# Kernel tuning notes

Measured on AMD Instinct MI355X. Metric: run time of the kernel, lower is better.

The kernel has to match this reference:

```python
import jax, jax.numpy as jnp
import numpy as np
from functools import partial

# ---- constants mirroring init_kwargs ----
T, B, J, I = 1024, 32, 128, 512
KD = 16              # max_delay (dilated kernel size)
THETA = 1.0          # threshold
SIG = 0.5            # delay.SIG, frozen (requires_grad=False)
ALPHA = 5.0          # ATan surrogate alpha
EPS = 1e-5           # BatchNorm eps

# ---- ATan surrogate spike (spikingjelly): fwd = heaviside, bwd = atan grad ----
@jax.custom_vjp
def atan_spike(x):
    return (x >= 0).astype(x.dtype)

def _atan_fwd(x):
    return atan_spike(x), x

def _atan_bwd(x, g):
    return (g * (ALPHA / 2.0) / (1.0 + (jnp.pi / 2.0 * ALPHA * x) ** 2),)

atan_spike.defvjp(_atan_fwd, _atan_bwd)

def _dcls_kernel(w, P):
    # DCLS1d 'gauss' version, kernel_count=1: gaussian bump centered at P + KD//2,
    # normalized over the kernel axis, scaled by weight. w,P: (I,J) -> (I,J,KD)
    c = P + KD // 2
    k = jnp.arange(KD, dtype=w.dtype)                        # (KD,)
    g = jnp.exp(-0.5 * ((k[None, None, :] - c[:, :, None]) / SIG) ** 2)
    g = g / (g.sum(-1, keepdims=True) + 1e-7)
    return w[:, :, None] * g                                  # (I,J,KD)

def setup_inputs() -> dict:
    key = jax.random.key(0)
    ks = jax.random.split(key, 6)
    x = jax.random.normal(ks[0], (T, B, J), dtype=jnp.float32)
    # kaiming_uniform_ fan_in = J*1 -> bound = sqrt(6/fan_in)
    bound = float(np.sqrt(6.0 / J))
    delay_w = jax.random.uniform(ks[1], (I, J), jnp.float32, -bound, bound)
    # P ~ U(-max_delay//2, max_delay//2), then clamped (already in range)
    delay_P = jax.random.uniform(ks[2], (I, J), jnp.float32, -(KD // 2), KD // 2)
    beta = jax.random.uniform(ks[3], (I,), jnp.float32, 0.0, 1.0)
    bn_gamma = jnp.ones((I,), jnp.float32)
    bn_beta = jnp.zeros((I,), jnp.float32)
    U0 = jax.random.uniform(ks[4], (B, I), jnp.float32)       # RandomBatchwiseInit(0,1)
    return {"x": x, "delay_w": delay_w, "delay_P": delay_P, "beta": beta,
            "bn_gamma": bn_gamma, "bn_beta": bn_beta, "U0": U0}

def reference(x, delay_w, delay_P, beta, bn_gamma, bn_beta, U0):
    # --- delayed conv: (T,B,J) -> (B,J,T) -> left-pad KD-1 -> conv1d -> (T,B,I) ---
    xb = jnp.transpose(x, (1, 2, 0))                          # (B,J,T)
    xb = jnp.pad(xb, ((0, 0), (0, 0), (KD - 1, 0)))           # (B,J,T+KD-1)
    kern = _dcls_kernel(delay_w, delay_P)                     # (I,J,KD)
    y = jax.lax.conv_general_dilated(
        xb, kern, window_strides=(1,), padding='VALID',
        dimension_numbers=('NCH', 'OIH', 'NCH'))              # (B,I,T)
    y = jnp.transpose(y, (2, 0, 1))                           # (T,B,I)

    # --- BatchNorm1d over reshaped (T*B, I, 1): stats over T*B per channel ---
    yf = y.reshape(T * B, I)
    mean = yf.mean(axis=0)
    var = yf.var(axis=0)
    yf = (yf - mean) * jax.lax.rsqrt(var + EPS) * bn_gamma + bn_beta
    y = yf.reshape(T, B, I)

    # --- soft-reset LIF scan (NOTE: original passes RAW beta, not sigmoid(beta)) ---
    def step(carry, xt):
        Ut, St = carry
        Ut = beta * (Ut - THETA * St) + (1.0 - beta) * xt
        St = atan_spike(Ut - THETA)
        return (Ut, St), St

    S0 = jnp.zeros_like(U0)
    _, o = jax.lax.scan(step, (U0, S0), y)                    # (T,B,I)
    return o
```

## Files before the change

### kernel.cpp

```cpp
#include <hip/hip_runtime.h>

#define TT 1024
#define NB 32
#define NJ 128
#define NI 512
#define KD 16
#define LVL 1048576

typedef short bf16x8 __attribute__((ext_vector_type(8)));
typedef float floatx4 __attribute__((ext_vector_type(4)));

struct S3 { short h, m, l; };

__device__ __forceinline__ S3 split3(float v) {
    S3 o;
    unsigned hb = __float_as_uint(v) & 0xFFFF0000u;
    float hf = __uint_as_float(hb);
    float r1 = v - hf;
    unsigned mb = __float_as_uint(r1) & 0xFFFF0000u;
    float mf = __uint_as_float(mb);
    float r2 = r1 - mf;
    unsigned lb = __float_as_uint(r2) & 0xFFFF0000u;
    o.h = (short)(hb >> 16);
    o.m = (short)(mb >> 16);
    o.l = (short)(lb >> 16);
    return o;
}

__global__ __launch_bounds__(256) void dcls_kern(const float* __restrict__ w,
                                                 const float* __restrict__ P,
                                                 short* __restrict__ WF) {
    int idx = blockIdx.x * 256 + threadIdx.x;
    int j = idx & (NJ - 1);
    int i = idx >> 7;
    float wv = w[i * NJ + j];
    float c  = P[i * NJ + j] + (float)(KD / 2);
    float g[KD];
    float s = 0.f;
#pragma unroll
    for (int k = 0; k < KD; ++k) {
        float u = (float)k - c;
        g[k] = expf(-2.0f * u * u);
        s += g[k];
    }
    float inv = wv / (s + 1e-7f);
    size_t base = (size_t)(i >> 4) * 32768 + (size_t)(j >> 3) * 128 + (i & 15) * 8 + (j & 7);
#pragma unroll
    for (int d = 0; d < KD; ++d) {
        S3 sp = split3(g[(KD - 1) - d] * inv);
        size_t off = base + (size_t)d * 2048;
        WF[off]           = sp.h;
        WF[off + LVL]     = sp.m;
        WF[off + 2 * LVL] = sp.l;
    }
}

__global__ __launch_bounds__(512, 2) void conv_mfma(const float* __restrict__ x,
                                                    const short* __restrict__ WF,
                                                    float* __restrict__ y) {
    __shared__ __align__(16) short PA[256][64];
    __shared__ __align__(16) short PL[256][64];

    const int t0 = blockIdx.x * 256;
    const int i0 = blockIdx.y * 256;
    const int b  = blockIdx.z;
    const int tid = threadIdx.x;

    const int ch   = tid & 3;
    const int rw   = tid >> 2;
    const int l    = tid & 63;
    const int wv   = tid >> 6;
    const int lr16 = l & 15;
    const int kb   = l >> 4;
    const int wm   = wv >> 2;
    const int wn   = wv & 3;

    const short* pnf[4];
#pragma unroll
    for (int nf = 0; nf < 4; ++nf) {
        int ig = (i0 + wn * 64 + nf * 16) >> 4;
        pnf[nf] = WF + (size_t)ig * 32768 + l * 8;
    }

    floatx4 acc[8][4];
#pragma unroll
    for (int mf = 0; mf < 8; ++mf)
#pragma unroll
        for (int nf = 0; nf < 4; ++nf)
#pragma unroll
            for (int e = 0; e < 4; ++e) acc[mf][nf][e] = 0.f;

    float4 ga[2][2];
    bf16x8 Wh[4], Wm[4], Wl[4];

#define LOADW(K) {                                                              \
    int koff = ((((K) >> 2) * 16 + ((K) & 3) * 4)) * 128;                       \
    _Pragma("unroll") for (int nf = 0; nf < 4; ++nf) {                          \
        const short* p = pnf[nf] + koff;                                        \
        Wh[nf] = *(const bf16x8*)(p);                                           \
        Wm[nf] = *(const bf16x8*)(p + LVL);                                     \
        Wl[nf] = *(const bf16x8*)(p + 2 * LVL); } }

#define LOADX(K) {                                                              \
    int dn = (K) >> 2, j0n = ((K) & 3) << 5;                                    \
    _Pragma("unroll") for (int s = 0; s < 2; ++s) {                             \
        int t = t0 + rw + s * 128 - dn;                                         \
        float4 z4 = make_float4(0.f, 0.f, 0.f, 0.f);                            \
        ga[s][0] = z4; ga[s][1] = z4;                                           \
        if (t >= 0) {                                                           \
            const float* ax = x + ((size_t)t * NB + b) * NJ + j0n + ch * 8;     \
            ga[s][0] = *(const float4*)ax;                                      \
            ga[s][1] = *(const float4*)(ax + 4); } } }

#define STAGEW() {                                                              \
    _Pragma("unroll") for (int s = 0; s < 2; ++s) {                             \
        int r = rw + s * 128;                                                   \
        int key = r & 7;                                                        \
        char* rowA = (char*)PA + r * 128;                                       \
        char* rowL = (char*)PL + r * 128;                                       \
        S3 a0 = split3(ga[s][0].x), a1 = split3(ga[s][0].y),                    \
           a2 = split3(ga[s][0].z), a3 = split3(ga[s][0].w),                    \
           a4 = split3(ga[s][1].x), a5 = split3(ga[s][1].y),                    \
           a6 = split3(ga[s][1].z), a7 = split3(ga[s][1].w);                    \
        bf16x8 h8, m8, l8;                                                      \
        h8[0]=a0.h; h8[1]=a1.h; h8[2]=a2.h; h8[3]=a3.h;                         \
        h8[4]=a4.h; h8[5]=a5.h; h8[6]=a6.h; h8[7]=a7.h;                         \
        m8[0]=a0.m; m8[1]=a1.m; m8[2]=a2.m; m8[3]=a3.m;                         \
        m8[4]=a4.m; m8[5]=a5.m; m8[6]=a6.m; m8[7]=a7.m;                         \
        l8[0]=a0.l; l8[1]=a1.l; l8[2]=a2.l; l8[3]=a3.l;                         \
        l8[4]=a4.l; l8[5]=a5.l; l8[6]=a6.l; l8[7]=a7.l;                         \
        *(bf16x8*)(rowA + ((ch ^ key) * 16))       = h8;                        \
        *(bf16x8*)(rowA + (((ch + 4) ^ key) * 16)) = m8;                        \
        *(bf16x8*)(rowL + ((ch ^ key) * 16))       = l8; } }

#define DOMFMA() {                                                              \
    _Pragma("unroll") for (int mf = 0; mf < 8; ++mf) {                          \
        int row = wm * 128 + mf * 16 + lr16;                                    \
        int key = row & 7;                                                      \
        const char* rowA = (const char*)PA + row * 128;                         \
        const char* rowL = (const char*)PL + row * 128;                         \
        bf16x8 ah = *(const bf16x8*)(rowA + ((kb ^ key) * 16));                 \
        bf16x8 am = *(const bf16x8*)(rowA + (((kb + 4) ^ key) * 16));           \
        bf16x8 al = *(const bf16x8*)(rowL + ((kb ^ key) * 16));                 \
        _Pragma("unroll") for (int nf = 0; nf < 4; ++nf)                        \
            acc[mf][nf] = __builtin_amdgcn_mfma_f32_16x16x32_bf16(ah, Wh[nf], acc[mf][nf], 0, 0, 0); \
        _Pragma("unroll") for (int nf = 0; nf < 4; ++nf)                        \
            acc[mf][nf] = __builtin_amdgcn_mfma_f32_16x16x32_bf16(ah, Wm[nf], acc[mf][nf], 0, 0, 0); \
        _Pragma("unroll") for (int nf = 0; nf < 4; ++nf)                        \
            acc[mf][nf] = __builtin_amdgcn_mfma_f32_16x16x32_bf16(am, Wh[nf], acc[mf][nf], 0, 0, 0); \
        _Pragma("unroll") for (int nf = 0; nf < 4; ++nf)                        \
            acc[mf][nf] = __builtin_amdgcn_mfma_f32_16x16x32_bf16(am, Wm[nf], acc[mf][nf], 0, 0, 0); \
        _Pragma("unroll") for (int nf = 0; nf < 4; ++nf)                        \
            acc[mf][nf] = __builtin_amdgcn_mfma_f32_16x16x32_bf16(ah, Wl[nf], acc[mf][nf], 0, 0, 0); \
        _Pragma("unroll") for (int nf = 0; nf < 4; ++nf)                        \
            acc[mf][nf] = __builtin_amdgcn_mfma_f32_16x16x32_bf16(al, Wh[nf], acc[mf][nf], 0, 0, 0); \
    } }

    LOADX(0)

#pragma unroll 1
    for (int kk = 0; kk < 64; ++kk) {
        __syncthreads();
        STAGEW()
        __syncthreads();
        if (kk + 1 < 64) { LOADX(kk + 1) }
        LOADW(kk)
        DOMFMA()
    }
#undef LOADW
#undef LOADX
#undef STAGEW
#undef DOMFMA

#pragma unroll
    for (int mf = 0; mf < 8; ++mf)
#pragma unroll
        for (int nf = 0; nf < 4; ++nf) {
            int ic = i0 + wn * 64 + nf * 16 + lr16;
#pragma unroll
            for (int q = 0; q < 4; ++q) {
                int t = t0 + wm * 128 + mf * 16 + kb * 4 + q;
                y[((size_t)t * NB + b) * NI + ic] = acc[mf][nf][q];
            }
        }
}

__global__ __launch_bounds__(256) void red1(const float* __restrict__ y,
                                            float* __restrict__ part) {
    int r0 = blockIdx.x * 128;
    int c  = threadIdx.x;
    float s0 = 0.f, q0 = 0.f, s1 = 0.f, q1 = 0.f;
#pragma unroll 4
    for (int r = 0; r < 128; ++r) {
        float v0 = y[(size_t)(r0 + r) * NI + c];
        float v1 = y[(size_t)(r0 + r) * NI + c + 256];
        s0 += v0; q0 = fmaf(v0, v0, q0);
        s1 += v1; q1 = fmaf(v1, v1, q1);
    }
    part[blockIdx.x * NI + c]            = s0;
    part[blockIdx.x * NI + c + 256]      = s1;
    part[256 * NI + blockIdx.x * NI + c]       = q0;
    part[256 * NI + blockIdx.x * NI + c + 256] = q1;
}

__global__ __launch_bounds__(512) void red2(const float* __restrict__ part,
                                            const float* __restrict__ gamma,
                                            const float* __restrict__ bbeta,
                                            float* __restrict__ sb) {
    int c = threadIdx.x;
    double s = 0.0, q = 0.0;
#pragma unroll 8
    for (int p = 0; p < 256; ++p) {
        s += (double)part[p * NI + c];
        q += (double)part[256 * NI + p * NI + c];
    }
    double mean = s / 32768.0;
    double var  = q / 32768.0 - mean * mean;
    double scale = (double)gamma[c] / sqrt(var + 1e-5);
    sb[c]      = (float)scale;
    sb[NI + c] = (float)((double)bbeta[c] - mean * scale);
}

__global__ __launch_bounds__(64) void scan_kern(float* __restrict__ y,
                                                const float* __restrict__ sb,
                                                const float* __restrict__ beta,
                                                const float* __restrict__ U0) {
    int g = blockIdx.x * 64 + threadIdx.x;
    int i = g & (NI - 1);
    float scale = sb[i];
    float bias  = sb[NI + i];
    float bet = beta[i];
    float omb = 1.f - bet;
    float u = U0[g];
    float s = 0.f;
    float* yp = y + g;

    float A[32], Bv[32];
#pragma unroll
    for (int r = 0; r < 32; ++r) A[r] = yp[(size_t)r * 16384];

    for (int t0 = 0; t0 < TT; t0 += 64) {
#pragma unroll
        for (int r = 0; r < 32; ++r) Bv[r] = yp[(size_t)(t0 + 32 + r) * 16384];
#pragma unroll
        for (int r = 0; r < 32; ++r) {
            float z = fmaf(A[r], scale, bias);
            u = fmaf(bet, u - s, omb * z);
            s = (u >= 1.f) ? 1.f : 0.f;
            yp[(size_t)(t0 + r) * 16384] = s;
        }
        if (t0 + 64 < TT) {
#pragma unroll
            for (int r = 0; r < 32; ++r) A[r] = yp[(size_t)(t0 + 64 + r) * 16384];
        }
#pragma unroll
        for (int r = 0; r < 32; ++r) {
            float z = fmaf(Bv[r], scale, bias);
            u = fmaf(bet, u - s, omb * z);
            s = (u >= 1.f) ? 1.f : 0.f;
            yp[(size_t)(t0 + 32 + r) * 16384] = s;
        }
    }
}

extern "C" void kernel_launch(void* const* d_in, const int* in_sizes, int n_in,
                              void* d_out, int out_size, void* d_ws, size_t ws_size,
                              hipStream_t stream) {
    const float* x       = (const float*)d_in[0];
    const float* delay_w = (const float*)d_in[1];
    const float* delay_P = (const float*)d_in[2];
    const float* beta    = (const float*)d_in[3];
    const float* bn_g    = (const float*)d_in[4];
    const float* bn_b    = (const float*)d_in[5];
    const float* U0      = (const float*)d_in[6];
    float* y = (float*)d_out;

    short* WF   = (short*)d_ws;
    float* part = (float*)d_ws;
    float* sb   = (float*)d_ws + 2 * 256 * NI;

    dcls_kern<<<dim3(NI * NJ / 256), dim3(256), 0, stream>>>(delay_w, delay_P, WF);
    conv_mfma<<<dim3(TT / 256, NI / 256, NB), dim3(512), 0, stream>>>(x, WF, y);
    red1<<<dim3(TT * NB / 128), dim3(256), 0, stream>>>(y, part);
    red2<<<dim3(1), dim3(512), 0, stream>>>(part, bn_g, bn_b, sb);
    scan_kern<<<dim3(NB * NI / 64), dim3(64), 0, stream>>>(y, sb, beta, U0);
}
```

Before: 357.4 us.

## Double-buffer conv tiles via direct global-to-LDS loads on a pre-padded input

A new kernel copies x into a zero-padded buffer in workspace, so the conv kernel needs no boundary checks. The conv kernel then streams raw fp32 tiles straight into LDS with global_load_lds and double-buffers both the x tiles and the weight registers, overlapping loads with MFMA work. The three-way bf16 split of activations moves from the staging step to each MFMA read. This removes the register round-trip and one barrier per step, but repeats the split for every wave that reads a row and adds one extra kernel pass over x.

```diff
diff --git a/kernel.cpp b/kernel.cpp
--- a/kernel.cpp
+++ b/kernel.cpp
@@ -6,6 +6,8 @@
 #define NI 512
 #define KD 16
 #define LVL 1048576
+#define XPROWS 1039
+#define XPF4 1063936
 
 typedef short bf16x8 __attribute__((ext_vector_type(8)));
 typedef float floatx4 __attribute__((ext_vector_type(4)));
@@ -27,6 +29,12 @@
     return o;
 }
 
+__device__ __forceinline__ void gload16(const void* g, void* l) {
+    __builtin_amdgcn_global_load_lds(
+        (const __attribute__((address_space(1))) void*)g,
+        (__attribute__((address_space(3))) void*)l, 16, 0, 0);
+}
+
 __global__ __launch_bounds__(256) void dcls_kern(const float* __restrict__ w,
                                                  const float* __restrict__ P,
                                                  short* __restrict__ WF) {
@@ -55,19 +63,27 @@
     }
 }
 
-__global__ __launch_bounds__(512, 2) void conv_mfma(const float* __restrict__ x,
+__global__ __launch_bounds__(512) void pad_kern(const float* __restrict__ x,
+                                                float* __restrict__ xp) {
+    size_t i4 = (size_t)blockIdx.x * 512 + threadIdx.x;
+    if (i4 >= XPF4) return;
+    size_t off = i4 * 4;
+    float4 v = make_float4(0.f, 0.f, 0.f, 0.f);
+    if (off >= (size_t)15 * 4096) v = *(const float4*)(x + off - 61440);
+    *(float4*)(xp + off) = v;
+}
+
+__global__ __launch_bounds__(512, 2) void conv_mfma(const float* __restrict__ xpad,
                                                     const short* __restrict__ WF,
                                                     float* __restrict__ y) {
-    __shared__ __align__(16) short PA[256][64];
-    __shared__ __align__(16) short PL[256][64];
+    __shared__ __align__(16) float XT0[256][32];
+    __shared__ __align__(16) float XT1[256][32];
 
     const int t0 = blockIdx.x * 256;
     const int i0 = blockIdx.y * 256;
     const int b  = blockIdx.z;
     const int tid = threadIdx.x;
 
-    const int ch   = tid & 3;
-    const int rw   = tid >> 2;
     const int l    = tid & 63;
     const int wv   = tid >> 6;
     const int lr16 = l & 15;
@@ -75,6 +91,9 @@
     const int wm   = wv >> 2;
     const int wn   = wv & 3;
 
+    const int srow = tid >> 3;
+    const int gch  = (tid & 7) ^ ((tid >> 3) & 7);
+
     const short* pnf[4];
 #pragma unroll
     for (int nf = 0; nf < 4; ++nf) {
@@ -90,86 +109,72 @@
 #pragma unroll
             for (int e = 0; e < 4; ++e) acc[mf][nf][e] = 0.f;
 
-    float4 ga[2][2];
-    bf16x8 Wh[4], Wm[4], Wl[4];
-
-#define LOADW(K) {                                                              \
+    bf16x8 W0h[4], W0m[4], W0l[4], W1h[4], W1m[4], W1l[4];
+
+#define LOADW(K, H, M, L_) {                                                    \
     int koff = ((((K) >> 2) * 16 + ((K) & 3) * 4)) * 128;                       \
     _Pragma("unroll") for (int nf = 0; nf < 4; ++nf) {                          \
         const short* p = pnf[nf] + koff;                                        \
-        Wh[nf] = *(const bf16x8*)(p);                                           \
-        Wm[nf] = *(const bf16x8*)(p + LVL);                                     \
-        Wl[nf] = *(const bf16x8*)(p + 2 * LVL); } }
-
-#define LOADX(K) {                                                              \
+        H[nf]  = *(const bf16x8*)(p);                                           \
+        M[nf]  = *(const bf16x8*)(p + LVL);                                     \
+        L_[nf] = *(const bf16x8*)(p + 2 * LVL); } }
+
+#define GLOAD(K, TILE) {                                                        \
     int dn = (K) >> 2, j0n = ((K) & 3) << 5;                                    \
-    _Pragma("unroll") for (int s = 0; s < 2; ++s) {                             \
-        int t = t0 + rw + s * 128 - dn;                                         \
-        float4 z4 = make_float4(0.f, 0.f, 0.f, 0.f);                            \
-        ga[s][0] = z4; ga[s][1] = z4;                                           \
-        if (t >= 0) {                                                           \
-            const float* ax = x + ((size_t)t * NB + b) * NJ + j0n + ch * 8;     \
-            ga[s][0] = *(const float4*)ax;                                      \
-            ga[s][1] = *(const float4*)(ax + 4); } } }
-
-#define STAGEW() {                                                              \
-    _Pragma("unroll") for (int s = 0; s < 2; ++s) {                             \
-        int r = rw + s * 128;                                                   \
-        int key = r & 7;                                                        \
-        char* rowA = (char*)PA + r * 128;                                       \
-        char* rowL = (char*)PL + r * 128;                                       \
-        S3 a0 = split3(ga[s][0].x), a1 = split3(ga[s][0].y),                    \
-           a2 = split3(ga[s][0].z), a3 = split3(ga[s][0].w),                    \
-           a4 = split3(ga[s][1].x), a5 = split3(ga[s][1].y),                    \
-           a6 = split3(ga[s][1].z), a7 = split3(ga[s][1].w);                    \
-        bf16x8 h8, m8, l8;                                                      \
-        h8[0]=a0.h; h8[1]=a1.h; h8[2]=a2.h; h8[3]=a3.h;                         \
-        h8[4]=a4.h; h8[5]=a5.h; h8[6]=a6.h; h8[7]=a7.h;                         \
-        m8[0]=a0.m; m8[1]=a1.m; m8[2]=a2.m; m8[3]=a3.m;                         \
-        m8[4]=a4.m; m8[5]=a5.m; m8[6]=a6.m; m8[7]=a7.m;                         \
-        l8[0]=a0.l; l8[1]=a1.l; l8[2]=a2.l; l8[3]=a3.l;                         \
-        l8[4]=a4.l; l8[5]=a5.l; l8[6]=a6.l; l8[7]=a7.l;                         \
-        *(bf16x8*)(rowA + ((ch ^ key) * 16))       = h8;                        \
-        *(bf16x8*)(rowA + (((ch + 4) ^ key) * 16)) = m8;                        \
-        *(bf16x8*)(rowL + ((ch ^ key) * 16))       = l8; } }
-
-#define DOMFMA() {                                                              \
+    _Pragma("unroll") for (int q = 0; q < 4; ++q) {                             \
+        int r  = q * 64 + srow;                                                 \
+        int tp = t0 + r - dn + 15;                                              \
+        const float* src = xpad + ((size_t)tp * NB + b) * NJ + j0n + gch * 4;   \
+        gload16(src, (char*)&TILE[0][0] + q * 8192 + tid * 16); } }
+
+#define DOMFMA(TILE, WH, WM, WL) {                                              \
     _Pragma("unroll") for (int mf = 0; mf < 8; ++mf) {                          \
         int row = wm * 128 + mf * 16 + lr16;                                    \
-        int key = row & 7;                                                      \
-        const char* rowA = (const char*)PA + row * 128;                         \
-        const char* rowL = (const char*)PL + row * 128;                         \
-        bf16x8 ah = *(const bf16x8*)(rowA + ((kb ^ key) * 16));                 \
-        bf16x8 am = *(const bf16x8*)(rowA + (((kb + 4) ^ key) * 16));           \
-        bf16x8 al = *(const bf16x8*)(rowL + ((kb ^ key) * 16));                 \
-        _Pragma("unroll") for (int nf = 0; nf < 4; ++nf)                        \
-            acc[mf][nf] = __builtin_amdgcn_mfma_f32_16x16x32_bf16(ah, Wh[nf], acc[mf][nf], 0, 0, 0); \
-        _Pragma("unroll") for (int nf = 0; nf < 4; ++nf)                        \
-            acc[mf][nf] = __builtin_amdgcn_mfma_f32_16x16x32_bf16(ah, Wm[nf], acc[mf][nf], 0, 0, 0); \
-        _Pragma("unroll") for (int nf = 0; nf < 4; ++nf)                        \
-            acc[mf][nf] = __builtin_amdgcn_mfma_f32_16x16x32_bf16(am, Wh[nf], acc[mf][nf], 0, 0, 0); \
-        _Pragma("unroll") for (int nf = 0; nf < 4; ++nf)                        \
-            acc[mf][nf] = __builtin_amdgcn_mfma_f32_16x16x32_bf16(am, Wm[nf], acc[mf][nf], 0, 0, 0); \
-        _Pragma("unroll") for (int nf = 0; nf < 4; ++nf)                        \
-            acc[mf][nf] = __builtin_amdgcn_mfma_f32_16x16x32_bf16(ah, Wl[nf], acc[mf][nf], 0, 0, 0); \
-        _Pragma("unroll") for (int nf = 0; nf < 4; ++nf)                        \
-            acc[mf][nf] = __builtin_amdgcn_mfma_f32_16x16x32_bf16(al, Wh[nf], acc[mf][nf], 0, 0, 0); \
+        int key = lr16 & 7;                                                     \
+        const float* rp = &TILE[row][0];                                        \
+        int c0 = (((2 * kb)     ^ key) << 2);                                   \
+        int c1 = (((2 * kb + 1) ^ key) << 2);                                   \
+        float4 fa = *(const float4*)(rp + c0);                                  \
+        float4 fb = *(const float4*)(rp + c1);                                  \
+        S3 s0 = split3(fa.x), s1 = split3(fa.y), s2 = split3(fa.z),             \
+           s3 = split3(fa.w), s4 = split3(fb.x), s5 = split3(fb.y),             \
+           s6 = split3(fb.z), s7 = split3(fb.w);                                \
+        bf16x8 ah, am, al;                                                      \
+        ah[0]=s0.h; ah[1]=s1.h; ah[2]=s2.h; ah[3]=s3.h;                         \
+        ah[4]=s4.h; ah[5]=s5.h; ah[6]=s6.h; ah[7]=s7.h;                         \
+        am[0]=s0.m; am[1]=s1.m; am[2]=s2.m; am[3]=s3.m;                         \
+        am[4]=s4.m; am[5]=s5.m; am[6]=s6.m; am[7]=s7.m;                         \
+        al[0]=s0.l; al[1]=s1.l; al[2]=s2.l; al[3]=s3.l;                         \
+        al[4]=s4.l; al[5]=s5.l; al[6]=s6.l; al[7]=s7.l;                         \
+        _Pragma("unroll") for (int nf = 0; nf < 4; ++nf)                        \
+            acc[mf][nf] = __builtin_amdgcn_mfma_f32_16x16x32_bf16(ah, WH[nf], acc[mf][nf], 0, 0, 0); \
+        _Pragma("unroll") for (int nf = 0; nf < 4; ++nf)                        \
+            acc[mf][nf] = __builtin_amdgcn_mfma_f32_16x16x32_bf16(ah, WM[nf], acc[mf][nf], 0, 0, 0); \
+        _Pragma("unroll") for (int nf = 0; nf < 4; ++nf)                        \
+            acc[mf][nf] = __builtin_amdgcn_mfma_f32_16x16x32_bf16(am, WH[nf], acc[mf][nf], 0, 0, 0); \
+        _Pragma("unroll") for (int nf = 0; nf < 4; ++nf)                        \
+            acc[mf][nf] = __builtin_amdgcn_mfma_f32_16x16x32_bf16(am, WM[nf], acc[mf][nf], 0, 0, 0); \
+        _Pragma("unroll") for (int nf = 0; nf < 4; ++nf)                        \
+            acc[mf][nf] = __builtin_amdgcn_mfma_f32_16x16x32_bf16(ah, WL[nf], acc[mf][nf], 0, 0, 0); \
+        _Pragma("unroll") for (int nf = 0; nf < 4; ++nf)                        \
+            acc[mf][nf] = __builtin_amdgcn_mfma_f32_16x16x32_bf16(al, WH[nf], acc[mf][nf], 0, 0, 0); \
     } }
 
-    LOADX(0)
+    GLOAD(0, XT0)
+    LOADW(0, W0h, W0m, W0l)
+    __syncthreads();
 
 #pragma unroll 1
-    for (int kk = 0; kk < 64; ++kk) {
+    for (int kk = 0; kk < 64; kk += 2) {
+        if (kk + 1 < 64) { GLOAD(kk + 1, XT1) LOADW(kk + 1, W1h, W1m, W1l) }
+        DOMFMA(XT0, W0h, W0m, W0l)
         __syncthreads();
-        STAGEW()
+        if (kk + 2 < 64) { GLOAD(kk + 2, XT0) LOADW(kk + 2, W0h, W0m, W0l) }
+        if (kk + 1 < 64) { DOMFMA(XT1, W1h, W1m, W1l) }
         __syncthreads();
-        if (kk + 1 < 64) { LOADX(kk + 1) }
-        LOADW(kk)
-        DOMFMA()
     }
 #undef LOADW
-#undef LOADX
-#undef STAGEW
+#undef GLOAD
 #undef DOMFMA
 
 #pragma unroll
@@ -276,11 +281,13 @@
     float* y = (float*)d_out;
 
     short* WF   = (short*)d_ws;
+    float* xpad = (float*)d_ws + 3 * (size_t)LVL / 2;
     float* part = (float*)d_ws;
     float* sb   = (float*)d_ws + 2 * 256 * NI;
 
     dcls_kern<<<dim3(NI * NJ / 256), dim3(256), 0, stream>>>(delay_w, delay_P, WF);
-    conv_mfma<<<dim3(TT / 256, NI / 256, NB), dim3(512), 0, stream>>>(x, WF, y);
+    pad_kern<<<dim3((XPF4 + 511) / 512), dim3(512), 0, stream>>>(x, xpad);
+    conv_mfma<<<dim3(TT / 256, NI / 256, NB), dim3(512), 0, stream>>>(xpad, WF, y);
     red1<<<dim3(TT * NB / 128), dim3(256), 0, stream>>>(y, part);
     red2<<<dim3(1), dim3(512), 0, stream>>>(part, bn_g, bn_b, sb);
     scan_kern<<<dim3(NB * NI / 64), dim3(64), 0, stream>>>(y, sb, beta, U0);
```

Result: slower. 392.1 us (+9.7%).

## Double-buffer conv LDS tiles and weight registers with interleaved staging

Applied to the files above, without the earlier changes.

Restructures the conv MFMA main loop into a software pipeline. The LDS A/L tiles and the weight register fragments are double-buffered, and the staging of the next tile, the weight loads and the x loads are interleaved between groups of MFMAs. This cuts the two barriers per iteration to one and hides global and LDS latency behind compute. The L tile also uses an 80-byte padded row in place of the XOR swizzle. In exchange the kernel needs 104 KB of dynamic LDS, which may allow only one block per CU where the launch bounds ask for two, and it holds twice as many weight registers.

```diff
diff --git a/kernel.cpp b/kernel.cpp
--- a/kernel.cpp
+++ b/kernel.cpp
@@ -58,8 +58,10 @@
 __global__ __launch_bounds__(512, 2) void conv_mfma(const float* __restrict__ x,
                                                     const short* __restrict__ WF,
                                                     float* __restrict__ y) {
-    __shared__ __align__(16) short PA[256][64];
-    __shared__ __align__(16) short PL[256][64];
+    extern __shared__ __align__(16) char lds[];
+    char* PAb[2]; char* PLb[2];
+    PAb[0] = lds;            PAb[1] = lds + 32768;
+    PLb[0] = lds + 65536;    PLb[1] = lds + 86016;
 
     const int t0 = blockIdx.x * 256;
     const int i0 = blockIdx.y * 256;
@@ -91,15 +93,15 @@
             for (int e = 0; e < 4; ++e) acc[mf][nf][e] = 0.f;
 
     float4 ga[2][2];
-    bf16x8 Wh[4], Wm[4], Wl[4];
-
-#define LOADW(K) {                                                              \
+    bf16x8 W0h[4], W0m[4], W0l[4], W1h[4], W1m[4], W1l[4];
+
+#define LOADW(K, H, M, L_) {                                                    \
     int koff = ((((K) >> 2) * 16 + ((K) & 3) * 4)) * 128;                       \
     _Pragma("unroll") for (int nf = 0; nf < 4; ++nf) {                          \
         const short* p = pnf[nf] + koff;                                        \
-        Wh[nf] = *(const bf16x8*)(p);                                           \
-        Wm[nf] = *(const bf16x8*)(p + LVL);                                     \
-        Wl[nf] = *(const bf16x8*)(p + 2 * LVL); } }
+        H[nf]  = *(const bf16x8*)(p);                                           \
+        M[nf]  = *(const bf16x8*)(p + LVL);                                     \
+        L_[nf] = *(const bf16x8*)(p + 2 * LVL); } }
 
 #define LOADX(K) {                                                              \
     int dn = (K) >> 2, j0n = ((K) & 3) << 5;                                    \
@@ -112,65 +114,77 @@
             ga[s][0] = *(const float4*)ax;                                      \
             ga[s][1] = *(const float4*)(ax + 4); } } }
 
-#define STAGEW() {                                                              \
-    _Pragma("unroll") for (int s = 0; s < 2; ++s) {                             \
-        int r = rw + s * 128;                                                   \
-        int key = r & 7;                                                        \
-        char* rowA = (char*)PA + r * 128;                                       \
-        char* rowL = (char*)PL + r * 128;                                       \
-        S3 a0 = split3(ga[s][0].x), a1 = split3(ga[s][0].y),                    \
-           a2 = split3(ga[s][0].z), a3 = split3(ga[s][0].w),                    \
-           a4 = split3(ga[s][1].x), a5 = split3(ga[s][1].y),                    \
-           a6 = split3(ga[s][1].z), a7 = split3(ga[s][1].w);                    \
-        bf16x8 h8, m8, l8;                                                      \
-        h8[0]=a0.h; h8[1]=a1.h; h8[2]=a2.h; h8[3]=a3.h;                         \
-        h8[4]=a4.h; h8[5]=a5.h; h8[6]=a6.h; h8[7]=a7.h;                         \
-        m8[0]=a0.m; m8[1]=a1.m; m8[2]=a2.m; m8[3]=a3.m;                         \
-        m8[4]=a4.m; m8[5]=a5.m; m8[6]=a6.m; m8[7]=a7.m;                         \
-        l8[0]=a0.l; l8[1]=a1.l; l8[2]=a2.l; l8[3]=a3.l;                         \
-        l8[4]=a4.l; l8[5]=a5.l; l8[6]=a6.l; l8[7]=a7.l;                         \
-        *(bf16x8*)(rowA + ((ch ^ key) * 16))       = h8;                        \
-        *(bf16x8*)(rowA + (((ch + 4) ^ key) * 16)) = m8;                        \
-        *(bf16x8*)(rowL + ((ch ^ key) * 16))       = l8; } }
-
-#define DOMFMA() {                                                              \
-    _Pragma("unroll") for (int mf = 0; mf < 8; ++mf) {                          \
+#define STAGE_ROW(S, BA, BL) {                                                  \
+    int r = rw + (S) * 128;                                                     \
+    int key = r & 7;                                                            \
+    char* rowA = (BA) + r * 128;                                                \
+    char* rowL = (BL) + r * 80;                                                 \
+    S3 a0 = split3(ga[S][0].x), a1 = split3(ga[S][0].y),                        \
+       a2 = split3(ga[S][0].z), a3 = split3(ga[S][0].w),                        \
+       a4 = split3(ga[S][1].x), a5 = split3(ga[S][1].y),                        \
+       a6 = split3(ga[S][1].z), a7 = split3(ga[S][1].w);                        \
+    bf16x8 h8, m8, l8;                                                          \
+    h8[0]=a0.h; h8[1]=a1.h; h8[2]=a2.h; h8[3]=a3.h;                             \
+    h8[4]=a4.h; h8[5]=a5.h; h8[6]=a6.h; h8[7]=a7.h;                             \
+    m8[0]=a0.m; m8[1]=a1.m; m8[2]=a2.m; m8[3]=a3.m;                             \
+    m8[4]=a4.m; m8[5]=a5.m; m8[6]=a6.m; m8[7]=a7.m;                             \
+    l8[0]=a0.l; l8[1]=a1.l; l8[2]=a2.l; l8[3]=a3.l;                             \
+    l8[4]=a4.l; l8[5]=a5.l; l8[6]=a6.l; l8[7]=a7.l;                             \
+    *(bf16x8*)(rowA + ((ch ^ key) * 16))       = h8;                            \
+    *(bf16x8*)(rowA + (((ch + 4) ^ key) * 16)) = m8;                            \
+    *(bf16x8*)(rowL + ch * 16)                 = l8; }
+
+#define DOQUAD(Q, BA, BL, WH, WM, WL) {                                         \
+    _Pragma("unroll") for (int mf = 2 * (Q); mf < 2 * (Q) + 2; ++mf) {          \
         int row = wm * 128 + mf * 16 + lr16;                                    \
         int key = row & 7;                                                      \
-        const char* rowA = (const char*)PA + row * 128;                         \
-        const char* rowL = (const char*)PL + row * 128;                         \
+        const char* rowA = (const char*)(BA) + row * 128;                       \
+        const char* rowL = (const char*)(BL) + row * 80;                        \
         bf16x8 ah = *(const bf16x8*)(rowA + ((kb ^ key) * 16));                 \
         bf16x8 am = *(const bf16x8*)(rowA + (((kb + 4) ^ key) * 16));           \
-        bf16x8 al = *(const bf16x8*)(rowL + ((kb ^ key) * 16));                 \
-        _Pragma("unroll") for (int nf = 0; nf < 4; ++nf)                        \
-            acc[mf][nf] = __builtin_amdgcn_mfma_f32_16x16x32_bf16(ah, Wh[nf], acc[mf][nf], 0, 0, 0); \
-        _Pragma("unroll") for (int nf = 0; nf < 4; ++nf)                        \
-            acc[mf][nf] = __builtin_amdgcn_mfma_f32_16x16x32_bf16(ah, Wm[nf], acc[mf][nf], 0, 0, 0); \
-        _Pragma("unroll") for (int nf = 0; nf < 4; ++nf)                        \
-            acc[mf][nf] = __builtin_amdgcn_mfma_f32_16x16x32_bf16(am, Wh[nf], acc[mf][nf], 0, 0, 0); \
-        _Pragma("unroll") for (int nf = 0; nf < 4; ++nf)                        \
-            acc[mf][nf] = __builtin_amdgcn_mfma_f32_16x16x32_bf16(am, Wm[nf], acc[mf][nf], 0, 0, 0); \
-        _Pragma("unroll") for (int nf = 0; nf < 4; ++nf)                        \
-            acc[mf][nf] = __builtin_amdgcn_mfma_f32_16x16x32_bf16(ah, Wl[nf], acc[mf][nf], 0, 0, 0); \
-        _Pragma("unroll") for (int nf = 0; nf < 4; ++nf)                        \
-            acc[mf][nf] = __builtin_amdgcn_mfma_f32_16x16x32_bf16(al, Wh[nf], acc[mf][nf], 0, 0, 0); \
+        bf16x8 al = *(const bf16x8*)(rowL + kb * 16);                           \
+        _Pragma("unroll") for (int nf = 0; nf < 4; ++nf)                        \
+            acc[mf][nf] = __builtin_amdgcn_mfma_f32_16x16x32_bf16(ah, WH[nf], acc[mf][nf], 0, 0, 0); \
+        _Pragma("unroll") for (int nf = 0; nf < 4; ++nf)                        \
+            acc[mf][nf] = __builtin_amdgcn_mfma_f32_16x16x32_bf16(ah, WM[nf], acc[mf][nf], 0, 0, 0); \
+        _Pragma("unroll") for (int nf = 0; nf < 4; ++nf)                        \
+            acc[mf][nf] = __builtin_amdgcn_mfma_f32_16x16x32_bf16(am, WH[nf], acc[mf][nf], 0, 0, 0); \
+        _Pragma("unroll") for (int nf = 0; nf < 4; ++nf)                        \
+            acc[mf][nf] = __builtin_amdgcn_mfma_f32_16x16x32_bf16(am, WM[nf], acc[mf][nf], 0, 0, 0); \
+        _Pragma("unroll") for (int nf = 0; nf < 4; ++nf)                        \
+            acc[mf][nf] = __builtin_amdgcn_mfma_f32_16x16x32_bf16(ah, WL[nf], acc[mf][nf], 0, 0, 0); \
+        _Pragma("unroll") for (int nf = 0; nf < 4; ++nf)                        \
+            acc[mf][nf] = __builtin_amdgcn_mfma_f32_16x16x32_bf16(al, WH[nf], acc[mf][nf], 0, 0, 0); \
     } }
 
+#define STEP(K, BC_A, BC_L, BN_A, BN_L, WCh, WCm, WCl, WNh, WNm, WNl) {         \
+    DOQUAD(0, BC_A, BC_L, WCh, WCm, WCl)                                        \
+    if ((K) + 1 < 64) { STAGE_ROW(0, BN_A, BN_L) }                              \
+    DOQUAD(1, BC_A, BC_L, WCh, WCm, WCl)                                        \
+    if ((K) + 1 < 64) { LOADW((K) + 1, WNh, WNm, WNl) }                         \
+    DOQUAD(2, BC_A, BC_L, WCh, WCm, WCl)                                        \
+    if ((K) + 1 < 64) { STAGE_ROW(1, BN_A, BN_L) }                              \
+    if ((K) + 2 < 64) { LOADX((K) + 2) }                                        \
+    DOQUAD(3, BC_A, BC_L, WCh, WCm, WCl)                                        \
+    __syncthreads(); }
+
     LOADX(0)
+    STAGE_ROW(0, PAb[0], PLb[0])
+    STAGE_ROW(1, PAb[0], PLb[0])
+    LOADX(1)
+    LOADW(0, W0h, W0m, W0l)
+    __syncthreads();
 
 #pragma unroll 1
-    for (int kk = 0; kk < 64; ++kk) {
-        __syncthreads();
-        STAGEW()
-        __syncthreads();
-        if (kk + 1 < 64) { LOADX(kk + 1) }
-        LOADW(kk)
-        DOMFMA()
+    for (int kk = 0; kk < 64; kk += 2) {
+        STEP(kk,     PAb[0], PLb[0], PAb[1], PLb[1], W0h, W0m, W0l, W1h, W1m, W1l)
+        STEP(kk + 1, PAb[1], PLb[1], PAb[0], PLb[0], W1h, W1m, W1l, W0h, W0m, W0l)
     }
 #undef LOADW
 #undef LOADX
-#undef STAGEW
-#undef DOMFMA
+#undef STAGE_ROW
+#undef DOQUAD
+#undef STEP
 
 #pragma unroll
     for (int mf = 0; mf < 8; ++mf)
@@ -279,8 +293,11 @@
     float* part = (float*)d_ws;
     float* sb   = (float*)d_ws + 2 * 256 * NI;
 
+    (void)hipFuncSetAttribute((const void*)conv_mfma,
+                              hipFuncAttributeMaxDynamicSharedMemorySize, 106496);
+
     dcls_kern<<<dim3(NI * NJ / 256), dim3(256), 0, stream>>>(delay_w, delay_P, WF);
-    conv_mfma<<<dim3(TT / 256, NI / 256, NB), dim3(512), 0, stream>>>(x, WF, y);
+    conv_mfma<<<dim3(TT / 256, NI / 256, NB), dim3(512), 106496, stream>>>(x, WF, y);
     red1<<<dim3(TT * NB / 128), dim3(256), 0, stream>>>(y, part);
     red2<<<dim3(1), dim3(512), 0, stream>>>(part, bn_g, bn_b, sb);
     scan_kern<<<dim3(NB * NI / 64), dim3(64), 0, stream>>>(y, sb, beta, U0);
```

Result: slower. 627.9 us (+75.7%).

## Switch conv GEMM from 16x16x32 to 32x32x16 bf16 MFMA tiles

Applied to the files above, without the earlier changes.

Replaces the 16x16x32 bf16 MFMA tiling in the split-precision conv GEMM with 32x32x16 MFMAs. The pre-split weight buffer layout is reorganised to match the 32-lane B-operand fragments, and the LDS A-fragment reads and output scatter are remapped to match. Larger MFMA tiles cut the number of LDS A-fragment reads and instructions per FLOP. The accumulator count per thread is unchanged, so register pressure stays about the same.

```diff
diff --git a/kernel.cpp b/kernel.cpp
--- a/kernel.cpp
+++ b/kernel.cpp
@@ -8,7 +8,7 @@
 #define LVL 1048576
 
 typedef short bf16x8 __attribute__((ext_vector_type(8)));
-typedef float floatx4 __attribute__((ext_vector_type(4)));
+typedef float floatx16 __attribute__((ext_vector_type(16)));
 
 struct S3 { short h, m, l; };
 
@@ -44,11 +44,12 @@
         s += g[k];
     }
     float inv = wv / (s + 1e-7f);
-    size_t base = (size_t)(i >> 4) * 32768 + (size_t)(j >> 3) * 128 + (i & 15) * 8 + (j & 7);
+    int lane = ((j >> 3) & 1) * 32 + (i & 31);
+    size_t base = (size_t)(i >> 5) * 65536 + (size_t)(j >> 4) * 512 + lane * 8 + (j & 7);
 #pragma unroll
     for (int d = 0; d < KD; ++d) {
         S3 sp = split3(g[(KD - 1) - d] * inv);
-        size_t off = base + (size_t)d * 2048;
+        size_t off = base + (size_t)d * 4096;
         WF[off]           = sp.h;
         WF[off + LVL]     = sp.m;
         WF[off + 2 * LVL] = sp.l;
@@ -70,36 +71,36 @@
     const int rw   = tid >> 2;
     const int l    = tid & 63;
     const int wv   = tid >> 6;
-    const int lr16 = l & 15;
-    const int kb   = l >> 4;
+    const int l31  = l & 31;
+    const int lhi  = l >> 5;
     const int wm   = wv >> 2;
     const int wn   = wv & 3;
 
-    const short* pnf[4];
-#pragma unroll
-    for (int nf = 0; nf < 4; ++nf) {
-        int ig = (i0 + wn * 64 + nf * 16) >> 4;
-        pnf[nf] = WF + (size_t)ig * 32768 + l * 8;
-    }
-
-    floatx4 acc[8][4];
-#pragma unroll
-    for (int mf = 0; mf < 8; ++mf)
-#pragma unroll
-        for (int nf = 0; nf < 4; ++nf)
-#pragma unroll
-            for (int e = 0; e < 4; ++e) acc[mf][nf][e] = 0.f;
+    const short* pnf[2];
+#pragma unroll
+    for (int nf = 0; nf < 2; ++nf) {
+        int ig = (i0 + wn * 64 + nf * 32) >> 5;
+        pnf[nf] = WF + (size_t)ig * 65536 + l * 8;
+    }
+
+    floatx16 acc[4][2];
+#pragma unroll
+    for (int mr = 0; mr < 4; ++mr)
+#pragma unroll
+        for (int nf = 0; nf < 2; ++nf)
+#pragma unroll
+            for (int e = 0; e < 16; ++e) acc[mr][nf][e] = 0.f;
 
     float4 ga[2][2];
-    bf16x8 Wh[4], Wm[4], Wl[4];
+    bf16x8 Bh[2][2], Bm[2][2], Bl[2][2];
 
 #define LOADW(K) {                                                              \
-    int koff = ((((K) >> 2) * 16 + ((K) & 3) * 4)) * 128;                       \
-    _Pragma("unroll") for (int nf = 0; nf < 4; ++nf) {                          \
-        const short* p = pnf[nf] + koff;                                        \
-        Wh[nf] = *(const bf16x8*)(p);                                           \
-        Wm[nf] = *(const bf16x8*)(p + LVL);                                     \
-        Wl[nf] = *(const bf16x8*)(p + 2 * LVL); } }
+    _Pragma("unroll") for (int nf = 0; nf < 2; ++nf)                            \
+    _Pragma("unroll") for (int ks = 0; ks < 2; ++ks) {                          \
+        const short* p = pnf[nf] + ((size_t)((K) * 2 + ks)) * 512;              \
+        Bh[nf][ks] = *(const bf16x8*)(p);                                       \
+        Bm[nf][ks] = *(const bf16x8*)(p + LVL);                                 \
+        Bl[nf][ks] = *(const bf16x8*)(p + 2 * LVL); } }
 
 #define LOADX(K) {                                                              \
     int dn = (K) >> 2, j0n = ((K) & 3) << 5;                                    \
@@ -134,27 +135,24 @@
         *(bf16x8*)(rowL + ((ch ^ key) * 16))       = l8; } }
 
 #define DOMFMA() {                                                              \
-    _Pragma("unroll") for (int mf = 0; mf < 8; ++mf) {                          \
-        int row = wm * 128 + mf * 16 + lr16;                                    \
+    _Pragma("unroll") for (int mr = 0; mr < 4; ++mr) {                          \
+        int row = wm * 128 + mr * 32 + l31;                                     \
         int key = row & 7;                                                      \
         const char* rowA = (const char*)PA + row * 128;                         \
         const char* rowL = (const char*)PL + row * 128;                         \
-        bf16x8 ah = *(const bf16x8*)(rowA + ((kb ^ key) * 16));                 \
-        bf16x8 am = *(const bf16x8*)(rowA + (((kb + 4) ^ key) * 16));           \
-        bf16x8 al = *(const bf16x8*)(rowL + ((kb ^ key) * 16));                 \
-        _Pragma("unroll") for (int nf = 0; nf < 4; ++nf)                        \
-            acc[mf][nf] = __builtin_amdgcn_mfma_f32_16x16x32_bf16(ah, Wh[nf], acc[mf][nf], 0, 0, 0); \
-        _Pragma("unroll") for (int nf = 0; nf < 4; ++nf)                        \
-            acc[mf][nf] = __builtin_amdgcn_mfma_f32_16x16x32_bf16(ah, Wm[nf], acc[mf][nf], 0, 0, 0); \
-        _Pragma("unroll") for (int nf = 0; nf < 4; ++nf)                        \
-            acc[mf][nf] = __builtin_amdgcn_mfma_f32_16x16x32_bf16(am, Wh[nf], acc[mf][nf], 0, 0, 0); \
-        _Pragma("unroll") for (int nf = 0; nf < 4; ++nf)                        \
-            acc[mf][nf] = __builtin_amdgcn_mfma_f32_16x16x32_bf16(am, Wm[nf], acc[mf][nf], 0, 0, 0); \
-        _Pragma("unroll") for (int nf = 0; nf < 4; ++nf)                        \
-            acc[mf][nf] = __builtin_amdgcn_mfma_f32_16x16x32_bf16(ah, Wl[nf], acc[mf][nf], 0, 0, 0); \
-        _Pragma("unroll") for (int nf = 0; nf < 4; ++nf)                        \
-            acc[mf][nf] = __builtin_amdgcn_mfma_f32_16x16x32_bf16(al, Wh[nf], acc[mf][nf], 0, 0, 0); \
-    } }
+        _Pragma("unroll") for (int ks = 0; ks < 2; ++ks) {                      \
+            int oct = ks * 2 + lhi;                                             \
+            bf16x8 ah = *(const bf16x8*)(rowA + ((oct ^ key) * 16));            \
+            bf16x8 am = *(const bf16x8*)(rowA + (((oct + 4) ^ key) * 16));      \
+            bf16x8 al = *(const bf16x8*)(rowL + ((oct ^ key) * 16));            \
+            _Pragma("unroll") for (int nf = 0; nf < 2; ++nf) {                  \
+                acc[mr][nf] = __builtin_amdgcn_mfma_f32_32x32x16_bf16(ah, Bh[nf][ks], acc[mr][nf], 0, 0, 0); \
+                acc[mr][nf] = __builtin_amdgcn_mfma_f32_32x32x16_bf16(ah, Bm[nf][ks], acc[mr][nf], 0, 0, 0); \
+                acc[mr][nf] = __builtin_amdgcn_mfma_f32_32x32x16_bf16(am, Bh[nf][ks], acc[mr][nf], 0, 0, 0); \
+                acc[mr][nf] = __builtin_amdgcn_mfma_f32_32x32x16_bf16(am, Bm[nf][ks], acc[mr][nf], 0, 0, 0); \
+                acc[mr][nf] = __builtin_amdgcn_mfma_f32_32x32x16_bf16(ah, Bl[nf][ks], acc[mr][nf], 0, 0, 0); \
+                acc[mr][nf] = __builtin_amdgcn_mfma_f32_32x32x16_bf16(al, Bh[nf][ks], acc[mr][nf], 0, 0, 0); \
+            } } } }
 
     LOADX(0)
 
@@ -173,15 +171,17 @@
 #undef DOMFMA
 
 #pragma unroll
-    for (int mf = 0; mf < 8; ++mf)
-#pragma unroll
-        for (int nf = 0; nf < 4; ++nf) {
-            int ic = i0 + wn * 64 + nf * 16 + lr16;
-#pragma unroll
-            for (int q = 0; q < 4; ++q) {
-                int t = t0 + wm * 128 + mf * 16 + kb * 4 + q;
-                y[((size_t)t * NB + b) * NI + ic] = acc[mf][nf][q];
-            }
+    for (int mr = 0; mr < 4; ++mr)
+#pragma unroll
+        for (int nf = 0; nf < 2; ++nf) {
+            int ic = i0 + wn * 64 + nf * 32 + l31;
+#pragma unroll
+            for (int g = 0; g < 4; ++g)
+#pragma unroll
+                for (int q = 0; q < 4; ++q) {
+                    int t = t0 + wm * 128 + mr * 32 + q + g * 8 + 4 * lhi;
+                    y[((size_t)t * NB + b) * NI + ic] = acc[mr][nf][g * 4 + q];
+                }
         }
 }
 
```

After: 384.0 us. +7.4%, slower.
